# Performance work log

Hardware: AMD Instinct MI355X
Metric: run time of the kernel (lower is better)

The kernel has to match this reference:

```python
import jax, jax.numpy as jnp
import numpy as np

B, S, DIN, DOUT = 4, 2048, 4096, 4096
QMAX = 127  # 2**(8-1) - 1


def setup_inputs() -> dict:
    key = jax.random.key(0)
    k_x, k_w, k_b, k_ws = jax.random.split(key, 4)
    x = jax.random.normal(k_x, (B, S, DIN), dtype=jnp.float32)
    # int8-valued weights stored as int32 (as in the torch module's .int() weight)
    weight = jax.random.randint(k_w, (DOUT, DIN), -QMAX, QMAX + 1, dtype=jnp.int32)
    bias = jax.random.randint(k_b, (DOUT,), -10, 11, dtype=jnp.int32)
    # per-input-channel weight scale, shape (out_features, 1)
    weight_scale = (jax.random.uniform(k_ws, (DOUT, 1), dtype=jnp.float32) * 0.01 + 1e-4)
    input_scale = jnp.float32(0.02)
    output_scale = jnp.float32(0.05)
    return {
        "x": x,
        "weight": weight,
        "bias": bias,
        "weight_scale": weight_scale,
        "input_scale": input_scale,
        "output_scale": output_scale,
    }


def reference(x, weight, bias, weight_scale, input_scale, output_scale):
    # fake-quantize activations: round to int grid, then dequantize back to float
    xq = jnp.round(x / input_scale).astype(jnp.int32).astype(jnp.float32) * input_scale
    # dequantize weights: (O, I)
    w = weight.astype(jnp.float32) * weight_scale
    # fp32 GEMM: [B,S,I] x [I,O] -> [B,S,O]
    ret = jnp.einsum("bsi,oi->bso", xq, w)
    ret = ret + bias.astype(jnp.float32)
    # requantize output to int grid (int32 output, as in torch .int())
    return jnp.round(ret / output_scale).astype(jnp.int32)
```

## Files before the change

### kernel.cpp

```cpp
#include <hip/hip_runtime.h>
#include <stdint.h>

#define MDIM 8192
#define KDIM 4096
#define NDIM 4096
#define BK   64
#define NKT  (KDIM / BK)

typedef float f32x4 __attribute__((ext_vector_type(4)));
typedef _Float16 h16x8 __attribute__((ext_vector_type(8)));
typedef short short8 __attribute__((ext_vector_type(8)));
typedef float fl4 __attribute__((ext_vector_type(4)));
typedef int i32x4 __attribute__((ext_vector_type(4)));

__device__ __forceinline__ void gload_lds16(const void* g, void* l) {
    __builtin_amdgcn_global_load_lds(
        (__attribute__((address_space(1))) void*)(uintptr_t)g,
        (__attribute__((address_space(3))) void*)(uintptr_t)l,
        16, 0, 0);
}

__global__ void __launch_bounds__(256) quant_kernel(const float* __restrict__ x,
                                                    short* __restrict__ xq,
                                                    const int* __restrict__ w,
                                                    short* __restrict__ wq,
                                                    const float* __restrict__ p_is) {
    if (blockIdx.x < 2048) {
        const float inv_is = 1.0f / p_is[0];
        const int64_t stride = (int64_t)2048 * 256 * 8;
        for (int64_t i = ((int64_t)blockIdx.x * 256 + threadIdx.x) * 8;
             i < (int64_t)MDIM * KDIM; i += stride) {
            fl4 a = __builtin_nontemporal_load((const fl4*)(x + i));
            fl4 b = __builtin_nontemporal_load((const fl4*)(x + i + 4));
            h16x8 o;
            o[0] = (_Float16)rintf(a[0] * inv_is);
            o[1] = (_Float16)rintf(a[1] * inv_is);
            o[2] = (_Float16)rintf(a[2] * inv_is);
            o[3] = (_Float16)rintf(a[3] * inv_is);
            o[4] = (_Float16)rintf(b[0] * inv_is);
            o[5] = (_Float16)rintf(b[1] * inv_is);
            o[6] = (_Float16)rintf(b[2] * inv_is);
            o[7] = (_Float16)rintf(b[3] * inv_is);
            *(h16x8*)(xq + i) = o;
        }
    } else {
        const int64_t stride = (int64_t)1024 * 256 * 8;
        for (int64_t i = (((int64_t)blockIdx.x - 2048) * 256 + threadIdx.x) * 8;
             i < (int64_t)NDIM * KDIM; i += stride) {
            i32x4 a = *(const i32x4*)(w + i);
            i32x4 b = *(const i32x4*)(w + i + 4);
            h16x8 o;
            o[0] = (_Float16)(float)a[0];
            o[1] = (_Float16)(float)a[1];
            o[2] = (_Float16)(float)a[2];
            o[3] = (_Float16)(float)a[3];
            o[4] = (_Float16)(float)b[0];
            o[5] = (_Float16)(float)b[1];
            o[6] = (_Float16)(float)b[2];
            o[7] = (_Float16)(float)b[3];
            *(h16x8*)(wq + i) = o;
        }
    }
}


#define PH_MID() do { \
    __builtin_amdgcn_s_barrier(); \
    asm volatile("s_waitcnt lgkmcnt(0)" ::: "memory"); \
    __builtin_amdgcn_sched_barrier(0); \
    __builtin_amdgcn_s_setprio(1); \
  } while (0)

#define PH_END() do { \
    __builtin_amdgcn_s_setprio(0); \
    __builtin_amdgcn_s_barrier(); \
    __builtin_amdgcn_sched_barrier(0); \
  } while (0)

#define PH_END_VM() do { \
    __builtin_amdgcn_s_setprio(0); \
    asm volatile("s_waitcnt vmcnt(4)" ::: "memory"); \
    __builtin_amdgcn_s_barrier(); \
    __builtin_amdgcn_sched_barrier(0); \
  } while (0)

__global__ void __launch_bounds__(512, 2) gemm_f16_kernel(
    const short* __restrict__ A,
    const short* __restrict__ Bw,
    const int* __restrict__ bias,
    const float* __restrict__ wscale,
    const float* __restrict__ p_is,
    const float* __restrict__ p_os,
    int* __restrict__ out) {
    __shared__ __align__(16) short lds[65536];

    const int tid  = threadIdx.x;
    const int lane = tid & 63;
    const int wave = tid >> 6;
    const int quad = lane >> 4;
    const int r16  = lane & 15;
    const int sw   = r16 & 7;

    const int flat  = blockIdx.y * gridDim.x + blockIdx.x;
    const int wgid  = (flat & 7) * 64 + (flat >> 3);
    const int m_blk = wgid >> 4;
    const int n_blk = wgid & 15;
    const int m0 = m_blk * 256;
    const int n0 = n_blk * 256;

    const int wmi = wave >> 2;
    const int wni = wave & 3;

    const int srow = tid >> 3;
    const int skc  = (tid & 7) ^ (srow & 7);
    const short* gA = A  + (int64_t)(m0 + srow) * KDIM + skc * 8;
    const short* gB = Bw + (int64_t)(n0 + srow) * KDIM + skc * 8;

#define STAGE_A(b, ha, T) do { \
    const short* _g = gA + (int64_t)((ha) * 128) * KDIM + (T) * BK; \
    gload_lds16(_g,             &lds[(b)*16384 + (ha)*8192 + wave*512]); \
    gload_lds16(_g + 64*KDIM,   &lds[(b)*16384 + (ha)*8192 + 4096 + wave*512]); \
  } while (0)
#define STAGE_B(b, ha, T) do { \
    const short* _g = gB + (int64_t)((ha) * 128) * KDIM + (T) * BK; \
    gload_lds16(_g,             &lds[32768 + (b)*16384 + (ha)*8192 + wave*512]); \
    gload_lds16(_g + 64*KDIM,   &lds[32768 + (b)*16384 + (ha)*8192 + 4096 + wave*512]); \
  } while (0)

    const int aRowOff = (wmi * 128 + r16) * 64;
    const int bRowOff = 32768 + (wni * 64 + r16) * 64;
    const int cOff0   = (quad ^ sw) * 8;
    const int cOff1   = cOff0 ^ 32;

#define LDA(b, mh, mi, ks) \
    (*(const h16x8*)&lds[(b)*16384 + aRowOff + ((mh)*64 + (mi)*16)*64 + ((ks) ? cOff1 : cOff0)])
#define LDB(b, nh, nj, ks) \
    (*(const h16x8*)&lds[(b)*16384 + bRowOff + ((nh)*32 + (nj)*16)*64 + ((ks) ? cOff1 : cOff0)])

#define READ_A(b, mh) do { \
    _Pragma("unroll") for (int mi = 0; mi < 4; ++mi) { \
        aR[mi][0] = LDA(b, mh, mi, 0); aR[mi][1] = LDA(b, mh, mi, 1); } \
  } while (0)
#define READ_B(b, nh, dst) do { \
    _Pragma("unroll") for (int nj = 0; nj < 2; ++nj) { \
        dst[nj][0] = LDB(b, nh, nj, 0); dst[nj][1] = LDB(b, nh, nj, 1); } \
  } while (0)
#define MFMA_Q(mh, nh, bsrc) do { \
    _Pragma("unroll") for (int mi = 0; mi < 4; ++mi) \
    _Pragma("unroll") for (int nj = 0; nj < 2; ++nj) \
    _Pragma("unroll") for (int ks = 0; ks < 2; ++ks) \
        acc[(mh)*4 + mi][(nh)*2 + nj] = __builtin_amdgcn_mfma_f32_16x16x32_f16( \
            aR[mi][ks], bsrc[nj][ks], acc[(mh)*4 + mi][(nh)*2 + nj], 0, 0, 0); \
  } while (0)

    f32x4 acc[8][4];
#pragma unroll
    for (int i = 0; i < 8; ++i)
#pragma unroll
        for (int j = 0; j < 4; ++j) acc[i][j] = (f32x4)0.0f;

    h16x8 aR[4][2], bLo[2][2], bHi[2][2];

    STAGE_A(0, 0, 0); STAGE_A(0, 1, 0);
    STAGE_B(0, 0, 0); STAGE_B(0, 1, 0);
    STAGE_B(1, 0, 1); STAGE_B(1, 1, 1);
    asm volatile("s_waitcnt vmcnt(4)" ::: "memory");
    __builtin_amdgcn_s_barrier();
    __builtin_amdgcn_sched_barrier(0);

    for (int it = 0; it < NKT / 2; ++it) {
        const int t1 = 2 * it + 1;
        const int tA = (2 * it + 2) & (NKT - 1);
        const int tB = (2 * it + 3) & (NKT - 1);

        READ_A(0, 0); READ_B(0, 0, bLo);
        STAGE_A(1, 0, t1);
        asm volatile("s_waitcnt lgkmcnt(8)" ::: "memory");
        PH_MID(); MFMA_Q(0, 0, bLo); PH_END();
        READ_B(0, 1, bHi);
        STAGE_A(1, 1, t1);
        PH_MID(); MFMA_Q(0, 1, bHi); PH_END();
        READ_A(0, 1);
        STAGE_B(0, 0, tA);
        PH_MID(); MFMA_Q(1, 1, bHi); PH_END();
        STAGE_B(0, 1, tA);
        PH_MID(); MFMA_Q(1, 0, bLo); PH_END_VM();
        READ_A(1, 0); READ_B(1, 0, bLo);
        STAGE_A(0, 0, tA);
        asm volatile("s_waitcnt lgkmcnt(8)" ::: "memory");
        PH_MID(); MFMA_Q(0, 0, bLo); PH_END();
        READ_B(1, 1, bHi);
        STAGE_A(0, 1, tA);
        PH_MID(); MFMA_Q(0, 1, bHi); PH_END();
        READ_A(1, 1);
        STAGE_B(1, 0, tB);
        PH_MID(); MFMA_Q(1, 1, bHi); PH_END();
        STAGE_B(1, 1, tB);
        PH_MID(); MFMA_Q(1, 0, bLo); PH_END_VM();
    }

    const float is = p_is[0];
    const float inv_os = 1.0f / p_os[0];
    const int colBase = n0 + wni * 64;

    float alpha[4], beta[4];
#pragma unroll
    for (int nj = 0; nj < 4; ++nj) {
        const int col = colBase + nj * 16 + r16;
        alpha[nj] = is * wscale[col] * inv_os;
        beta[nj]  = (float)bias[col] * inv_os;
    }

#pragma unroll
    for (int mi = 0; mi < 8; ++mi) {
        const int row0 = m0 + wmi * 128 + mi * 16 + quad * 4;
#pragma unroll
        for (int nj = 0; nj < 4; ++nj) {
            const int col = colBase + nj * 16 + r16;
#pragma unroll
            for (int reg = 0; reg < 4; ++reg) {
                const float v = acc[mi][nj][reg] * alpha[nj] + beta[nj];
                __builtin_nontemporal_store(__float2int_rn(v),
                                            out + (int64_t)(row0 + reg) * NDIM + col);
            }
        }
    }
}

extern "C" void kernel_launch(void* const* d_in, const int* in_sizes, int n_in,
                              void* d_out, int out_size, void* d_ws, size_t ws_size,
                              hipStream_t stream) {
    (void)in_sizes; (void)n_in; (void)out_size; (void)ws_size;
    const float* x      = (const float*)d_in[0];
    const int*   weight = (const int*)d_in[1];
    const int*   bias   = (const int*)d_in[2];
    const float* wscale = (const float*)d_in[3];
    const float* p_is   = (const float*)d_in[4];
    const float* p_os   = (const float*)d_in[5];

    short* xq = (short*)d_ws;
    short* wq = xq + (size_t)MDIM * KDIM;

    quant_kernel<<<3072, 256, 0, stream>>>(x, xq, weight, wq, p_is);

    dim3 grid(NDIM / 256, MDIM / 256);
    gemm_f16_kernel<<<grid, 512, 0, stream>>>(xq, wq, bias, wscale, p_is, p_os, (int*)d_out);
}
```

Before: 474.8 us.

## Fuse activation/weight quantization into GEMM loads, dropping separate quant kernel

Removes the standalone quantization pass that wrote fp16 copies of x and weight to workspace. The GEMM now loads fp32 activations and int32 weights into registers, converts them to fp16 (rounding activations), and writes them to LDS with ds_write instead of direct global-to-LDS loads. This saves a full read/write pass over both operands but doubles the bytes fetched per tile inside the GEMM. It also adds VALU conversion and register pressure, and loses the async LDS-load pipelining.

```diff
diff --git a/kernel.cpp b/kernel.cpp
--- a/kernel.cpp
+++ b/kernel.cpp
@@ -9,59 +9,8 @@
 
 typedef float f32x4 __attribute__((ext_vector_type(4)));
 typedef _Float16 h16x8 __attribute__((ext_vector_type(8)));
-typedef short short8 __attribute__((ext_vector_type(8)));
 typedef float fl4 __attribute__((ext_vector_type(4)));
 typedef int i32x4 __attribute__((ext_vector_type(4)));
-
-__device__ __forceinline__ void gload_lds16(const void* g, void* l) {
-    __builtin_amdgcn_global_load_lds(
-        (__attribute__((address_space(1))) void*)(uintptr_t)g,
-        (__attribute__((address_space(3))) void*)(uintptr_t)l,
-        16, 0, 0);
-}
-
-__global__ void __launch_bounds__(256) quant_kernel(const float* __restrict__ x,
-                                                    short* __restrict__ xq,
-                                                    const int* __restrict__ w,
-                                                    short* __restrict__ wq,
-                                                    const float* __restrict__ p_is) {
-    if (blockIdx.x < 2048) {
-        const float inv_is = 1.0f / p_is[0];
-        const int64_t stride = (int64_t)2048 * 256 * 8;
-        for (int64_t i = ((int64_t)blockIdx.x * 256 + threadIdx.x) * 8;
-             i < (int64_t)MDIM * KDIM; i += stride) {
-            fl4 a = __builtin_nontemporal_load((const fl4*)(x + i));
-            fl4 b = __builtin_nontemporal_load((const fl4*)(x + i + 4));
-            h16x8 o;
-            o[0] = (_Float16)rintf(a[0] * inv_is);
-            o[1] = (_Float16)rintf(a[1] * inv_is);
-            o[2] = (_Float16)rintf(a[2] * inv_is);
-            o[3] = (_Float16)rintf(a[3] * inv_is);
-            o[4] = (_Float16)rintf(b[0] * inv_is);
-            o[5] = (_Float16)rintf(b[1] * inv_is);
-            o[6] = (_Float16)rintf(b[2] * inv_is);
-            o[7] = (_Float16)rintf(b[3] * inv_is);
-            *(h16x8*)(xq + i) = o;
-        }
-    } else {
-        const int64_t stride = (int64_t)1024 * 256 * 8;
-        for (int64_t i = (((int64_t)blockIdx.x - 2048) * 256 + threadIdx.x) * 8;
-             i < (int64_t)NDIM * KDIM; i += stride) {
-            i32x4 a = *(const i32x4*)(w + i);
-            i32x4 b = *(const i32x4*)(w + i + 4);
-            h16x8 o;
-            o[0] = (_Float16)(float)a[0];
-            o[1] = (_Float16)(float)a[1];
-            o[2] = (_Float16)(float)a[2];
-            o[3] = (_Float16)(float)a[3];
-            o[4] = (_Float16)(float)b[0];
-            o[5] = (_Float16)(float)b[1];
-            o[6] = (_Float16)(float)b[2];
-            o[7] = (_Float16)(float)b[3];
-            *(h16x8*)(wq + i) = o;
-        }
-    }
-}
 
 
 #define PH_MID() do { \
@@ -77,16 +26,9 @@
     __builtin_amdgcn_sched_barrier(0); \
   } while (0)
 
-#define PH_END_VM() do { \
-    __builtin_amdgcn_s_setprio(0); \
-    asm volatile("s_waitcnt vmcnt(4)" ::: "memory"); \
-    __builtin_amdgcn_s_barrier(); \
-    __builtin_amdgcn_sched_barrier(0); \
-  } while (0)
-
-__global__ void __launch_bounds__(512, 2) gemm_f16_kernel(
-    const short* __restrict__ A,
-    const short* __restrict__ Bw,
+__global__ void __launch_bounds__(512, 2) gemm_fused_kernel(
+    const float* __restrict__ x,
+    const int* __restrict__ w,
     const int* __restrict__ bias,
     const float* __restrict__ wscale,
     const float* __restrict__ p_is,
@@ -101,6 +43,8 @@
     const int r16  = lane & 15;
     const int sw   = r16 & 7;
 
+    const float inv_is = 1.0f / p_is[0];
+
     const int flat  = blockIdx.y * gridDim.x + blockIdx.x;
     const int wgid  = (flat & 7) * 64 + (flat >> 3);
     const int m_blk = wgid >> 4;
@@ -113,19 +57,55 @@
 
     const int srow = tid >> 3;
     const int skc  = (tid & 7) ^ (srow & 7);
-    const short* gA = A  + (int64_t)(m0 + srow) * KDIM + skc * 8;
-    const short* gB = Bw + (int64_t)(n0 + srow) * KDIM + skc * 8;
-
-#define STAGE_A(b, ha, T) do { \
-    const short* _g = gA + (int64_t)((ha) * 128) * KDIM + (T) * BK; \
-    gload_lds16(_g,             &lds[(b)*16384 + (ha)*8192 + wave*512]); \
-    gload_lds16(_g + 64*KDIM,   &lds[(b)*16384 + (ha)*8192 + 4096 + wave*512]); \
-  } while (0)
-#define STAGE_B(b, ha, T) do { \
-    const short* _g = gB + (int64_t)((ha) * 128) * KDIM + (T) * BK; \
-    gload_lds16(_g,             &lds[32768 + (b)*16384 + (ha)*8192 + wave*512]); \
-    gload_lds16(_g + 64*KDIM,   &lds[32768 + (b)*16384 + (ha)*8192 + 4096 + wave*512]); \
-  } while (0)
+    const float* xg = x + (int64_t)(m0 + srow) * KDIM + skc * 8;
+    const int*   wg = w + (int64_t)(n0 + srow) * KDIM + skc * 8;
+
+#define DS_WRITE2(baseShorts, o1, o2) do { \
+    *(h16x8*)(&lds[(baseShorts) + tid * 8])        = (o1); \
+    *(h16x8*)(&lds[(baseShorts) + 4096 + tid * 8]) = (o2); \
+  } while (0)
+
+#define LOAD_A(v, ha, T) do { \
+    const float* _p = xg + (int64_t)((ha) * 128) * KDIM + (T) * BK; \
+    v[0] = *(const fl4*)_p;              v[1] = *(const fl4*)(_p + 4); \
+    v[2] = *(const fl4*)(_p + 64*KDIM);  v[3] = *(const fl4*)(_p + 64*KDIM + 4); \
+  } while (0)
+#define LOAD_B(v, ha, T) do { \
+    const int* _p = wg + (int64_t)((ha) * 128) * KDIM + (T) * BK; \
+    v[0] = *(const i32x4*)_p;             v[1] = *(const i32x4*)(_p + 4); \
+    v[2] = *(const i32x4*)(_p + 64*KDIM); v[3] = *(const i32x4*)(_p + 64*KDIM + 4); \
+  } while (0)
+
+#define CVT_A(o, p, q) do { \
+    o[0] = (_Float16)rintf(p[0] * inv_is); o[1] = (_Float16)rintf(p[1] * inv_is); \
+    o[2] = (_Float16)rintf(p[2] * inv_is); o[3] = (_Float16)rintf(p[3] * inv_is); \
+    o[4] = (_Float16)rintf(q[0] * inv_is); o[5] = (_Float16)rintf(q[1] * inv_is); \
+    o[6] = (_Float16)rintf(q[2] * inv_is); o[7] = (_Float16)rintf(q[3] * inv_is); \
+  } while (0)
+#define CVT_B(o, p, q) do { \
+    o[0] = (_Float16)(float)p[0]; o[1] = (_Float16)(float)p[1]; \
+    o[2] = (_Float16)(float)p[2]; o[3] = (_Float16)(float)p[3]; \
+    o[4] = (_Float16)(float)q[0]; o[5] = (_Float16)(float)q[1]; \
+    o[6] = (_Float16)(float)q[2]; o[7] = (_Float16)(float)q[3]; \
+  } while (0)
+
+#define WRITE_A(baseShorts, v) do { \
+    h16x8 _o1, _o2; CVT_A(_o1, v[0], v[1]); CVT_A(_o2, v[2], v[3]); \
+    DS_WRITE2(baseShorts, _o1, _o2); \
+  } while (0)
+#define WRITE_B(baseShorts, v) do { \
+    h16x8 _o1, _o2; CVT_B(_o1, v[0], v[1]); CVT_B(_o2, v[2], v[3]); \
+    DS_WRITE2(baseShorts, _o1, _o2); \
+  } while (0)
+
+#define A_B0H0 0
+#define A_B0H1 8192
+#define A_B1H0 16384
+#define A_B1H1 24576
+#define B_B0H0 32768
+#define B_B0H1 40960
+#define B_B1H0 49152
+#define B_B1H1 57344
 
     const int aRowOff = (wmi * 128 + r16) * 64;
     const int bRowOff = 32768 + (wni * 64 + r16) * 64;
@@ -160,43 +140,54 @@
         for (int j = 0; j < 4; ++j) acc[i][j] = (f32x4)0.0f;
 
     h16x8 aR[4][2], bLo[2][2], bHi[2][2];
-
-    STAGE_A(0, 0, 0); STAGE_A(0, 1, 0);
-    STAGE_B(0, 0, 0); STAGE_B(0, 1, 0);
-    STAGE_B(1, 0, 1); STAGE_B(1, 1, 1);
-    asm volatile("s_waitcnt vmcnt(4)" ::: "memory");
+    fl4   vA0[4], vA1[4];
+    i32x4 vB0[4], vB1[4];
+
+    LOAD_A(vA0, 0, 0); LOAD_A(vA1, 1, 0);
+    LOAD_B(vB0, 0, 0); LOAD_B(vB1, 1, 0);
+    WRITE_A(A_B0H0, vA0); WRITE_A(A_B0H1, vA1);
+    WRITE_B(B_B0H0, vB0); WRITE_B(B_B0H1, vB1);
+    LOAD_B(vB0, 0, 1); LOAD_B(vB1, 1, 1);
+    WRITE_B(B_B1H0, vB0); WRITE_B(B_B1H1, vB1);
+    LOAD_A(vA0, 0, 1); LOAD_A(vA1, 1, 1);
+    asm volatile("s_waitcnt lgkmcnt(0)" ::: "memory");
     __builtin_amdgcn_s_barrier();
     __builtin_amdgcn_sched_barrier(0);
 
     for (int it = 0; it < NKT / 2; ++it) {
-        const int t1 = 2 * it + 1;
         const int tA = (2 * it + 2) & (NKT - 1);
         const int tB = (2 * it + 3) & (NKT - 1);
 
         READ_A(0, 0); READ_B(0, 0, bLo);
-        STAGE_A(1, 0, t1);
-        asm volatile("s_waitcnt lgkmcnt(8)" ::: "memory");
+        WRITE_A(A_B1H0, vA0);
+        LOAD_B(vB0, 0, tA);
         PH_MID(); MFMA_Q(0, 0, bLo); PH_END();
         READ_B(0, 1, bHi);
-        STAGE_A(1, 1, t1);
+        WRITE_A(A_B1H1, vA1);
+        LOAD_B(vB1, 1, tA);
         PH_MID(); MFMA_Q(0, 1, bHi); PH_END();
         READ_A(0, 1);
-        STAGE_B(0, 0, tA);
+        WRITE_B(B_B0H0, vB0);
+        LOAD_A(vA0, 0, tA);
         PH_MID(); MFMA_Q(1, 1, bHi); PH_END();
-        STAGE_B(0, 1, tA);
-        PH_MID(); MFMA_Q(1, 0, bLo); PH_END_VM();
+        WRITE_B(B_B0H1, vB1);
+        LOAD_A(vA1, 1, tA);
+        PH_MID(); MFMA_Q(1, 0, bLo); PH_END();
         READ_A(1, 0); READ_B(1, 0, bLo);
-        STAGE_A(0, 0, tA);
-        asm volatile("s_waitcnt lgkmcnt(8)" ::: "memory");
+        WRITE_A(A_B0H0, vA0);
+        LOAD_B(vB0, 0, tB);
         PH_MID(); MFMA_Q(0, 0, bLo); PH_END();
         READ_B(1, 1, bHi);
-        STAGE_A(0, 1, tA);
+        WRITE_A(A_B0H1, vA1);
+        LOAD_B(vB1, 1, tB);
         PH_MID(); MFMA_Q(0, 1, bHi); PH_END();
         READ_A(1, 1);
-        STAGE_B(1, 0, tB);
+        WRITE_B(B_B1H0, vB0);
+        LOAD_A(vA0, 0, tB);
         PH_MID(); MFMA_Q(1, 1, bHi); PH_END();
-        STAGE_B(1, 1, tB);
-        PH_MID(); MFMA_Q(1, 0, bLo); PH_END_VM();
+        WRITE_B(B_B1H1, vB1);
+        LOAD_A(vA1, 1, tB);
+        PH_MID(); MFMA_Q(1, 0, bLo); PH_END();
     }
 
     const float is = p_is[0];
@@ -230,7 +221,7 @@
 extern "C" void kernel_launch(void* const* d_in, const int* in_sizes, int n_in,
                               void* d_out, int out_size, void* d_ws, size_t ws_size,
                               hipStream_t stream) {
-    (void)in_sizes; (void)n_in; (void)out_size; (void)ws_size;
+    (void)in_sizes; (void)n_in; (void)out_size; (void)d_ws; (void)ws_size;
     const float* x      = (const float*)d_in[0];
     const int*   weight = (const int*)d_in[1];
     const int*   bias   = (const int*)d_in[2];
@@ -238,11 +229,7 @@
     const float* p_is   = (const float*)d_in[4];
     const float* p_os   = (const float*)d_in[5];
 
-    short* xq = (short*)d_ws;
-    short* wq = xq + (size_t)MDIM * KDIM;
-
-    quant_kernel<<<3072, 256, 0, stream>>>(x, xq, weight, wq, p_is);
-
     dim3 grid(NDIM / 256, MDIM / 256);
-    gemm_f16_kernel<<<grid, 512, 0, stream>>>(xq, wq, bias, wscale, p_is, p_os, (int*)d_out);
+    gemm_fused_kernel<<<grid, 512, 0, stream>>>(x, weight, bias, wscale, p_is, p_os,
+                                                (int*)d_out);
 }
```

New measurement: 1.035 ms. 2.18x slower.
